# Performance work log

Hardware: AMD Instinct MI355X
Metric: run time of the kernel (lower is better)

## Reference

```python
import jax, jax.numpy as jnp
import numpy as np

N, T, D, H = 256, 512, 256, 256


def setup_inputs() -> dict:
    key = jax.random.key(0)
    ks = jax.random.split(key, 9)
    scale_x = float(np.sqrt(6.0 / (D + H)))  # xavier_uniform range approx
    scale_h = float(np.sqrt(6.0 / (H + H)))
    def wx(k):
        return jax.random.uniform(k, (D, H), jnp.float32, -scale_x, scale_x)
    def wh(k):
        return jax.random.uniform(k, (H, H), jnp.float32, -scale_h, scale_h)
    inp = {
        'x': jax.random.normal(ks[0], (N, T, D), jnp.float32),
        'w_ii': wx(ks[1]), 'w_hi': wh(ks[2]),
        'w_if': wx(ks[3]), 'w_hf': wh(ks[4]),
        'w_ig': wx(ks[5]), 'w_hg': wh(ks[6]),
        'w_io': wx(ks[7]), 'w_ho': wh(ks[8]),
        # init_hidden() zeros all 1-D params
        'b_ii': jnp.zeros((H,), jnp.float32), 'b_hi': jnp.zeros((H,), jnp.float32),
        'b_if': jnp.zeros((H,), jnp.float32), 'b_hf': jnp.zeros((H,), jnp.float32),
        'b_ig': jnp.zeros((H,), jnp.float32), 'b_hg': jnp.zeros((H,), jnp.float32),
        'b_io': jnp.zeros((H,), jnp.float32), 'b_ho': jnp.zeros((H,), jnp.float32),
    }
    return inp


def reference(x, w_ii, w_hi, w_if, w_hf, w_ig, w_hg, w_io, w_ho,
              b_ii, b_hi, b_if, b_hf, b_ig, b_hg, b_io, b_ho):
    # Fuse the 4 input projections and 4 hidden projections into 2 GEMMs
    # (mathematically identical to the 8 separate matmuls).
    Wx = jnp.concatenate([w_ii, w_if, w_ig, w_io], axis=1)  # (D, 4H)
    Wh = jnp.concatenate([w_hi, w_hf, w_hg, w_ho], axis=1)  # (H, 4H)
    b = jnp.concatenate([b_ii + b_hi, b_if + b_hf, b_ig + b_hg, b_io + b_ho])  # (4H,)
    n, t, _ = x.shape
    h = x.shape[2]  # noqa (not used)
    # Precompute input projections for all timesteps: (T, N, 4H)
    xW = jnp.einsum('ntd,dg->tng', x, Wx)
    h0 = jnp.zeros((n, w_hi.shape[0]), x.dtype)
    c0 = jnp.zeros_like(h0)

    def step(carry, xw_t):
        h_t, c_t = carry
        gates = xw_t + h_t @ Wh + b  # (N, 4H)
        i_t, f_t, g_t, o_t = jnp.split(gates, 4, axis=1)
        i_t = jax.nn.sigmoid(i_t)
        f_t = jax.nn.sigmoid(f_t)
        g_t = jnp.tanh(g_t)
        o_t = jax.nn.sigmoid(o_t)
        c_t = f_t * c_t + i_t * g_t
        h_t = o_t * jnp.tanh(c_t)
        return (h_t, c_t), None

    (h_T, c_T), _ = jax.lax.scan(step, (h0, c0), xW)
    return (h_T, c_T)
```

## Files before the change

kernel.cpp:

```cpp
#include <hip/hip_runtime.h>
#include <cstdint>

typedef float  f32x4  __attribute__((ext_vector_type(4)));
typedef __bf16 bf16x8 __attribute__((ext_vector_type(8)));
typedef int    i32x4  __attribute__((ext_vector_type(4)));
typedef unsigned short u16;
typedef u16 u16x4 __attribute__((ext_vector_type(4)));

#define TT 512

__device__ __forceinline__ u16 f2bf(float f) {
  unsigned u = __builtin_bit_cast(unsigned, f);
  unsigned r = u + 0x7fffu + ((u >> 16) & 1u);
  return (u16)(r >> 16);
}
__device__ __forceinline__ float bflo(unsigned d) { return __builtin_bit_cast(float, d << 16); }
__device__ __forceinline__ float bfhi(unsigned d) { return __builtin_bit_cast(float, d & 0xffff0000u); }
__device__ __forceinline__ float rcpf(float x) { return __builtin_amdgcn_rcpf(x); }
__device__ __forceinline__ float fsig(float x) { return rcpf(1.f + __expf(-x)); }
__device__ __forceinline__ float ftanh(float x) { return 1.f - 2.f * rcpf(1.f + __expf(2.f * x)); }
__device__ __forceinline__ void gload_lds16(const u16* g, u16* l) {
  __builtin_amdgcn_global_load_lds((const __attribute__((address_space(1))) void*)(g),
                                   (__attribute__((address_space(3))) void*)(l), 16, 0, 0);
}

__global__ __launch_bounds__(256) void prep_w(
    const float* __restrict__ wii, const float* __restrict__ whi,
    const float* __restrict__ wif, const float* __restrict__ whf,
    const float* __restrict__ wig, const float* __restrict__ whg,
    const float* __restrict__ wio, const float* __restrict__ who,
    const float* __restrict__ bii, const float* __restrict__ bhi,
    const float* __restrict__ bif, const float* __restrict__ bhf,
    const float* __restrict__ big_, const float* __restrict__ bhg,
    const float* __restrict__ bio, const float* __restrict__ bho,
    u16* __restrict__ Wxb, signed char* __restrict__ Whq,
    float* __restrict__ wscale, float* __restrict__ bsum) {
  __shared__ float red[256];
  int b = blockIdx.x;
  int tid = threadIdx.x;
  if (b < 1024) {
    const float* wx[4] = {wii, wif, wig, wio};
    int G = b >> 8, h = b & 255;
    Wxb[b * 256 + tid] = f2bf(wx[G][tid * 256 + h]);
  } else if (b < 2048) {
    const float* wh[4] = {whi, whf, whg, who};
    int cidx = b - 1024;
    int G = cidx >> 8, h = cidx & 255;
    float w = wh[G][tid * 256 + h];
    red[tid] = fabsf(w);
    __syncthreads();
    for (int s = 128; s > 0; s >>= 1) {
      if (tid < s) red[tid] = fmaxf(red[tid], red[tid + s]);
      __syncthreads();
    }
    float mx = red[0];
    float scale = (mx > 0.f) ? mx * (1.f / 127.f) : 1.f;
    float qf = rintf(w / scale);
    qf = fminf(127.f, fmaxf(-127.f, qf));
    Whq[cidx * 256 + tid] = (signed char)(int)qf;
    if (tid == 0) wscale[cidx] = scale * (1.f / 127.f);
  } else {
    const float* bx[4] = {bii, bif, big_, bio};
    const float* bh[4] = {bhi, bhf, bhg, bho};
    for (int G = 0; G < 4; ++G) bsum[G * 256 + tid] = bx[G][tid] + bh[G][tid];
  }
}

__global__ __launch_bounds__(256, 2) void gemm_xw(const float* __restrict__ X, const u16* __restrict__ Bt,
                                                  const float* __restrict__ bias, u16* __restrict__ xWp) {
  __shared__ u16 As[128 * 256];
  __shared__ u16 Bs[2][128 * 32];
  int bm = blockIdx.x;
  int tid = threadIdx.x;
  int l = tid & 63, w = tid >> 6;
  int wm = w >> 1, wn = w & 1;
  int c = l & 15, q = l >> 4;

  {
    int trow = tid >> 2, ch = tid & 3;
    gload_lds16(Bt + (size_t)trow * 256 + ch * 8, &Bs[0][0] + tid * 8);
    gload_lds16(Bt + (size_t)(trow + 64) * 256 + ch * 8, &Bs[0][0] + 2048 + tid * 8);
  }
  {
#pragma unroll 4
    for (int j = 0; j < 32; ++j) {
      int row_l = j * 4 + (tid >> 6);
      int d = (tid & 63) * 4;
      int r = bm * 128 + row_l;
      int t = r >> 8, n = r & 255;
      const float4 v = *(const float4*)(X + ((size_t)n * 512 + t) * 256 + d);
      u16x4 p;
      p[0] = f2bf(v.x); p[1] = f2bf(v.y); p[2] = f2bf(v.z); p[3] = f2bf(v.w);
      int ba = (row_l * 512 + d * 2) ^ ((row_l & 7) << 4);
      *(u16x4*)((char*)As + ba) = p;
    }
  }
  __syncthreads();

  f32x4 acc[4][4];
#pragma unroll
  for (int i = 0; i < 4; ++i)
#pragma unroll
    for (int j = 0; j < 4; ++j) acc[i][j] = (f32x4){0.f, 0.f, 0.f, 0.f};

  int sw = (c & 7) << 4;
  int rowbase[4];
#pragma unroll
  for (int mt = 0; mt < 4; ++mt)
    rowbase[mt] = (wm * 64 + mt * 16 + c) * 512;

  for (int bn = 0; bn < 8; ++bn) {
#pragma unroll
    for (int ko = 0; ko < 8; ++ko) {
      int sn = bn * 8 + ko + 1;
      if (sn < 64) {
        int bnn = sn >> 3, kon = sn & 7;
        const u16* Bb = Bt + (size_t)(bnn * 128) * 256 + kon * 32;
        u16* dst = &Bs[(ko + 1) & 1][0];
        int trow = tid >> 2, ch = tid & 3;
        gload_lds16(Bb + (size_t)trow * 256 + ch * 8, dst + tid * 8);
        gload_lds16(Bb + (size_t)(trow + 64) * 256 + ch * 8, dst + 2048 + tid * 8);
      }
      bf16x8 af[4], bfr[4];
      const u16* bp = &Bs[ko & 1][0];
      int koff = (ko * 64 + q * 16) ^ sw;
#pragma unroll
      for (int mt = 0; mt < 4; ++mt)
        af[mt] = *(const bf16x8*)((const char*)As + rowbase[mt] + koff);
#pragma unroll
      for (int nt = 0; nt < 4; ++nt)
        bfr[nt] = *(const bf16x8*)(bp + (wn * 64 + nt * 16 + c) * 32 + q * 8);
#pragma unroll
      for (int mt = 0; mt < 4; ++mt)
#pragma unroll
        for (int nt = 0; nt < 4; ++nt)
          acc[mt][nt] = __builtin_amdgcn_mfma_f32_16x16x32_bf16(af[mt], bfr[nt], acc[mt][nt], 0, 0, 0);
      __syncthreads();
    }
#pragma unroll
    for (int mt = 0; mt < 4; ++mt) {
      int tm = bm * 8 + wm * 4 + mt;
#pragma unroll
      for (int nt = 0; nt < 4; ++nt) {
        int tn = bn * 8 + wn * 4 + nt;
        float bv = bias[tn * 16 + c];
        u16x4 pk;
#pragma unroll
        for (int r = 0; r < 4; ++r) pk[r] = f2bf(acc[mt][nt][r] + bv);
        *reinterpret_cast<u16x4*>(xWp + ((size_t)(tm * 64 + tn) * 256 + l * 4)) = pk;
        acc[mt][nt] = (f32x4){0.f, 0.f, 0.f, 0.f};
      }
    }
  }
}

__global__ __launch_bounds__(512, 2) void lstm_rec(const signed char* __restrict__ Whq,
                                                   const float* __restrict__ wscale,
                                                   const u16* __restrict__ xWp,
                                                   float* __restrict__ out) {
  __shared__ __align__(16) signed char hb[2][576];
  int p = blockIdx.x;
  int xcd = p & 7, q8 = (p >> 3) & 7, tsel = p >> 6;
  int G = xcd * 2 + tsel;
  int tid = threadIdx.x;
  int wid = tid >> 6, l = tid & 63;
  int c = l & 15, q = (l >> 4) & 3;
  int tt = q >> 1, rsel = q & 1;

  for (int i = tid; i < 288; i += 512) ((int*)hb)[i] = 0;

  i32x4 bw[4][2][4];
#pragma unroll
  for (int g = 0; g < 4; ++g)
#pragma unroll
    for (int ttl = 0; ttl < 2; ++ttl) {
      int col = g * 256 + wid * 32 + ttl * 16 + c;
#pragma unroll
      for (int ks = 0; ks < 4; ++ks)
        bw[g][ttl][ks] = *reinterpret_cast<const i32x4*>(Whq + (size_t)col * 256 + ks * 64 + q * 16);
    }
  float sc8[4];
#pragma unroll
  for (int g = 0; g < 4; ++g) sc8[g] = wscale[g * 256 + wid * 32 + tt * 16 + c];

  const char* xbase = (const char*)xWp + (size_t)G * 32768;
  int xoff[4];
#pragma unroll
  for (int g = 0; g < 4; ++g) {
    int tn = g * 16 + wid * 2 + tt;
    xoff[g] = tn * 512 + (((q8 >> 1) * 16 + c) * 8) + (q8 & 1) * 4;
  }
  unsigned xw0[4], xw1[4];
#pragma unroll
  for (int g = 0; g < 4; ++g) xw0[g] = *(const unsigned*)(xbase + xoff[g]);
  xbase += 524288;

  i32x4 zacc = (i32x4){0, 0, 0, 0};
  float cs = 0.f, hh = 0.f;
  __syncthreads();

#define STEP(CUR, XW_CUR, XW_NXT)                                               \
  {                                                                             \
    _Pragma("unroll")                                                           \
    for (int g = 0; g < 4; ++g) XW_NXT[g] = *(const unsigned*)(xbase + xoff[g]);\
    const signed char* hr = hb[CUR ^ 1];                                        \
    i32x4 acc[4][2];                                                            \
    {                                                                           \
      i32x4 a0 = *(const i32x4*)(hr + (c & 1) * 288 + q * 16);                  \
      _Pragma("unroll")                                                         \
      for (int g = 0; g < 4; ++g) {                                             \
        __asm__("v_mfma_i32_16x16x64_i8 %0, %1, %2, %3"                         \
                : "=&v"(acc[g][0]) : "v"(a0), "a"(bw[g][0][0]), "v"(zacc));     \
        __asm__("v_mfma_i32_16x16x64_i8 %0, %1, %2, %3"                         \
                : "=&v"(acc[g][1]) : "v"(a0), "a"(bw[g][1][0]), "v"(zacc));     \
      }                                                                         \
    }                                                                           \
    _Pragma("unroll")                                                           \
    for (int ks = 1; ks < 4; ++ks) {                                            \
      i32x4 a = *(const i32x4*)(hr + (c & 1) * 288 + ks * 64 + q * 16);         \
      _Pragma("unroll")                                                         \
      for (int g = 0; g < 4; ++g) {                                             \
        __asm__("v_mfma_i32_16x16x64_i8 %0, %1, %2, %0"                         \
                : "+v"(acc[g][0]) : "v"(a), "a"(bw[g][0][ks]));                 \
        __asm__("v_mfma_i32_16x16x64_i8 %0, %1, %2, %0"                         \
                : "+v"(acc[g][1]) : "v"(a), "a"(bw[g][1][ks]));                 \
      }                                                                         \
    }                                                                           \
    __asm__ volatile("s_nop 7\n\ts_nop 7\n\ts_nop 7");   \
    float a4[4];                                                                \
    _Pragma("unroll")                                                           \
    for (int g = 0; g < 4; ++g) {                                               \
      int e = tt ? (rsel ? acc[g][1][1] : acc[g][1][0])                         \
                 : (rsel ? acc[g][0][1] : acc[g][0][0]);                        \
      unsigned d = XW_CUR[g];                                                   \
      float xv = rsel ? bfhi(d) : bflo(d);                                      \
      a4[g] = (float)e * sc8[g] + xv;                                           \
    }                                                                           \
    float gi = fsig(a4[0]);                                                     \
    float gf = fsig(a4[1]);                                                     \
    float gg = ftanh(a4[2]);                                                    \
    float go = fsig(a4[3]);                                                     \
    cs = gf * cs + gi * gg;                                                     \
    hh = go * ftanh(cs);                                                        \
    int hq = (int)rintf(hh * 127.f);                                            \
    hb[CUR][rsel * 288 + wid * 32 + tt * 16 + c] = (signed char)hq;             \
    xbase += 524288;                                                            \
    __builtin_amdgcn_s_waitcnt(0xC07F);   \
    __builtin_amdgcn_s_barrier();                                               \
  }

  for (int t = 0; t < TT; t += 2) {
    STEP(0, xw0, xw1)
    STEP(1, xw1, xw0)
  }
#undef STEP

  {
    int n = G * 16 + q8 * 2 + rsel;
    int hu = wid * 32 + tt * 16 + c;
    out[(size_t)n * 256 + hu] = hh;
    out[65536 + (size_t)n * 256 + hu] = cs;
  }
}

extern "C" void kernel_launch(void* const* d_in, const int* in_sizes, int n_in,
                              void* d_out, int out_size, void* d_ws, size_t ws_size,
                              hipStream_t stream) {
  const float* x   = (const float*)d_in[0];
  const float* wii = (const float*)d_in[1];
  const float* whi = (const float*)d_in[2];
  const float* wif = (const float*)d_in[3];
  const float* whf = (const float*)d_in[4];
  const float* wig = (const float*)d_in[5];
  const float* whg = (const float*)d_in[6];
  const float* wio = (const float*)d_in[7];
  const float* who = (const float*)d_in[8];
  const float* bii = (const float*)d_in[9];
  const float* bhi = (const float*)d_in[10];
  const float* bif = (const float*)d_in[11];
  const float* bhf = (const float*)d_in[12];
  const float* big_ = (const float*)d_in[13];
  const float* bhg = (const float*)d_in[14];
  const float* bio = (const float*)d_in[15];
  const float* bho = (const float*)d_in[16];

  char* ws = (char*)d_ws;
  u16*   Wxb    = (u16*)(ws + 67108864);
  signed char* Whq = (signed char*)(ws + 67633152);
  float* wscale = (float*)(ws + 67895296);
  float* bsum   = (float*)(ws + 67899392);
  u16*   xWp    = (u16*)(ws + 67903488);
  float* out = (float*)d_out;

  prep_w<<<2049, 256, 0, stream>>>(wii, whi, wif, whf, wig, whg, wio, who,
                                   bii, bhi, bif, bhf, big_, bhg, bio, bho,
                                   Wxb, Whq, wscale, bsum);
  gemm_xw<<<1024, 256, 0, stream>>>(x, Wxb, bsum, xWp);
  lstm_rec<<<128, 512, 0, stream>>>(Whq, wscale, xWp, out);
}
```

Baseline: 692.0 us.

## Fuse input GEMM and recurrence into one kernel with per-chunk progress flags

Merges the input-projection GEMM and the LSTM recurrence into a single launch. 128 blocks run the recurrence and 128 blocks compute xW in chunks of 64 timesteps, publishing completion through atomic counters. Recurrence blocks spin-wait on each chunk's counter before consuming it, so the GEMM overlaps with the serial recurrence instead of running before it. This relies on all 256 blocks being co-resident, adds spin-wait and barrier overhead, and gives the recurrence blocks the GEMM's large LDS footprint.

```diff
diff --git a/kernel.cpp b/kernel.cpp
--- a/kernel.cpp
+++ b/kernel.cpp
@@ -66,103 +66,103 @@
   }
 }
 
-__global__ __launch_bounds__(256, 2) void gemm_xw(const float* __restrict__ X, const u16* __restrict__ Bt,
-                                                  const float* __restrict__ bias, u16* __restrict__ xWp) {
+__global__ __launch_bounds__(512, 2) void lstm_fused(
+    const float* __restrict__ X, const u16* __restrict__ Bt,
+    const float* __restrict__ bias, const signed char* __restrict__ Whq,
+    const float* __restrict__ wscale, u16* __restrict__ xWp,
+    int* __restrict__ rprog, float* __restrict__ out) {
   __shared__ u16 As[128 * 256];
   __shared__ u16 Bs[2][128 * 32];
-  int bm = blockIdx.x;
-  int tid = threadIdx.x;
-  int l = tid & 63, w = tid >> 6;
-  int wm = w >> 1, wn = w & 1;
-  int c = l & 15, q = l >> 4;
-
-  {
-    int trow = tid >> 2, ch = tid & 3;
-    gload_lds16(Bt + (size_t)trow * 256 + ch * 8, &Bs[0][0] + tid * 8);
-    gload_lds16(Bt + (size_t)(trow + 64) * 256 + ch * 8, &Bs[0][0] + 2048 + tid * 8);
-  }
-  {
-#pragma unroll 4
-    for (int j = 0; j < 32; ++j) {
-      int row_l = j * 4 + (tid >> 6);
-      int d = (tid & 63) * 4;
-      int r = bm * 128 + row_l;
-      int t = r >> 8, n = r & 255;
-      const float4 v = *(const float4*)(X + ((size_t)n * 512 + t) * 256 + d);
-      u16x4 p;
-      p[0] = f2bf(v.x); p[1] = f2bf(v.y); p[2] = f2bf(v.z); p[3] = f2bf(v.w);
-      int ba = (row_l * 512 + d * 2) ^ ((row_l & 7) << 4);
-      *(u16x4*)((char*)As + ba) = p;
-    }
-  }
-  __syncthreads();
-
-  f32x4 acc[4][4];
-#pragma unroll
-  for (int i = 0; i < 4; ++i)
-#pragma unroll
-    for (int j = 0; j < 4; ++j) acc[i][j] = (f32x4){0.f, 0.f, 0.f, 0.f};
-
-  int sw = (c & 7) << 4;
-  int rowbase[4];
-#pragma unroll
-  for (int mt = 0; mt < 4; ++mt)
-    rowbase[mt] = (wm * 64 + mt * 16 + c) * 512;
-
-  for (int bn = 0; bn < 8; ++bn) {
-#pragma unroll
-    for (int ko = 0; ko < 8; ++ko) {
-      int sn = bn * 8 + ko + 1;
-      if (sn < 64) {
-        int bnn = sn >> 3, kon = sn & 7;
-        const u16* Bb = Bt + (size_t)(bnn * 128) * 256 + kon * 32;
-        u16* dst = &Bs[(ko + 1) & 1][0];
-        int trow = tid >> 2, ch = tid & 3;
-        gload_lds16(Bb + (size_t)trow * 256 + ch * 8, dst + tid * 8);
-        gload_lds16(Bb + (size_t)(trow + 64) * 256 + ch * 8, dst + 2048 + tid * 8);
-      }
-      bf16x8 af[4], bfr[4];
-      const u16* bp = &Bs[ko & 1][0];
-      int koff = (ko * 64 + q * 16) ^ sw;
-#pragma unroll
-      for (int mt = 0; mt < 4; ++mt)
-        af[mt] = *(const bf16x8*)((const char*)As + rowbase[mt] + koff);
-#pragma unroll
-      for (int nt = 0; nt < 4; ++nt)
-        bfr[nt] = *(const bf16x8*)(bp + (wn * 64 + nt * 16 + c) * 32 + q * 8);
-#pragma unroll
-      for (int mt = 0; mt < 4; ++mt)
-#pragma unroll
-        for (int nt = 0; nt < 4; ++nt)
-          acc[mt][nt] = __builtin_amdgcn_mfma_f32_16x16x32_bf16(af[mt], bfr[nt], acc[mt][nt], 0, 0, 0);
-      __syncthreads();
-    }
-#pragma unroll
-    for (int mt = 0; mt < 4; ++mt) {
-      int tm = bm * 8 + wm * 4 + mt;
-#pragma unroll
-      for (int nt = 0; nt < 4; ++nt) {
-        int tn = bn * 8 + wn * 4 + nt;
-        float bv = bias[tn * 16 + c];
-        u16x4 pk;
-#pragma unroll
-        for (int r = 0; r < 4; ++r) pk[r] = f2bf(acc[mt][nt][r] + bv);
-        *reinterpret_cast<u16x4*>(xWp + ((size_t)(tm * 64 + tn) * 256 + l * 4)) = pk;
-        acc[mt][nt] = (f32x4){0.f, 0.f, 0.f, 0.f};
-      }
-    }
-  }
-}
-
-__global__ __launch_bounds__(512, 2) void lstm_rec(const signed char* __restrict__ Whq,
-                                                   const float* __restrict__ wscale,
-                                                   const u16* __restrict__ xWp,
-                                                   float* __restrict__ out) {
   __shared__ __align__(16) signed char hb[2][576];
   int p = blockIdx.x;
+  int tid = threadIdx.x;
+
+  if (p >= 128) {
+    int k = p - 128;
+    int l = tid & 63, w8 = tid >> 6;
+    int wm = w8 >> 2, wn = w8 & 3;
+    int c = l & 15, q = l >> 4;
+    int sw = (c & 7) << 4;
+    int rowbase[4];
+#pragma unroll
+    for (int mt = 0; mt < 4; ++mt) rowbase[mt] = (wm * 64 + mt * 16 + c) * 512;
+
+    for (int j = 0; j < 8; ++j) {
+      int bm = j * 128 + k;
+      {
+        int trow = tid >> 2, ch = tid & 3;
+        gload_lds16(Bt + (size_t)trow * 256 + ch * 8, &Bs[0][0] + tid * 8);
+      }
+#pragma unroll 4
+      for (int jj = 0; jj < 16; ++jj) {
+        int row_l = jj * 8 + w8;
+        int d = l * 4;
+        int r = bm * 128 + row_l;
+        int t = r >> 8, n = r & 255;
+        const float4 v = *(const float4*)(X + ((size_t)n * 512 + t) * 256 + d);
+        u16x4 pk;
+        pk[0] = f2bf(v.x); pk[1] = f2bf(v.y); pk[2] = f2bf(v.z); pk[3] = f2bf(v.w);
+        int ba = (row_l * 512 + l * 8) ^ ((row_l & 7) << 4);
+        *(u16x4*)((char*)As + ba) = pk;
+      }
+      __syncthreads();
+
+      f32x4 acc[4][2];
+#pragma unroll
+      for (int i = 0; i < 4; ++i)
+#pragma unroll
+        for (int jn = 0; jn < 2; ++jn) acc[i][jn] = (f32x4){0.f, 0.f, 0.f, 0.f};
+
+      for (int bn = 0; bn < 8; ++bn) {
+#pragma unroll
+        for (int ko = 0; ko < 8; ++ko) {
+          int sn = bn * 8 + ko + 1;
+          if (sn < 64) {
+            int bnn = sn >> 3, kon = sn & 7;
+            const u16* Bb = Bt + (size_t)(bnn * 128) * 256 + kon * 32;
+            int trow = tid >> 2, ch = tid & 3;
+            gload_lds16(Bb + (size_t)trow * 256 + ch * 8, &Bs[(ko + 1) & 1][0] + tid * 8);
+          }
+          bf16x8 af[4], bfr[2];
+          const u16* bp = &Bs[ko & 1][0];
+          int koff = (ko * 64 + q * 16) ^ sw;
+#pragma unroll
+          for (int mt = 0; mt < 4; ++mt)
+            af[mt] = *(const bf16x8*)((const char*)As + rowbase[mt] + koff);
+#pragma unroll
+          for (int nt = 0; nt < 2; ++nt)
+            bfr[nt] = *(const bf16x8*)(bp + (wn * 32 + nt * 16 + c) * 32 + q * 8);
+#pragma unroll
+          for (int mt = 0; mt < 4; ++mt)
+#pragma unroll
+            for (int nt = 0; nt < 2; ++nt)
+              acc[mt][nt] = __builtin_amdgcn_mfma_f32_16x16x32_bf16(af[mt], bfr[nt], acc[mt][nt], 0, 0, 0);
+          __syncthreads();
+        }
+#pragma unroll
+        for (int mt = 0; mt < 4; ++mt) {
+          int tm = bm * 8 + wm * 4 + mt;
+#pragma unroll
+          for (int nt = 0; nt < 2; ++nt) {
+            int tn = bn * 8 + wn * 2 + nt;
+            float bv = bias[tn * 16 + c];
+            u16x4 pk;
+#pragma unroll
+            for (int r = 0; r < 4; ++r) pk[r] = f2bf(acc[mt][nt][r] + bv);
+            *reinterpret_cast<u16x4*>(xWp + ((size_t)(tm * 64 + tn) * 256 + l * 4)) = pk;
+            acc[mt][nt] = (f32x4){0.f, 0.f, 0.f, 0.f};
+          }
+        }
+      }
+      __syncthreads();
+      if (tid == 0)
+        __hip_atomic_fetch_add(&rprog[j], 1, __ATOMIC_RELEASE, __HIP_MEMORY_SCOPE_AGENT);
+    }
+    return;
+  }
+
   int xcd = p & 7, q8 = (p >> 3) & 7, tsel = p >> 6;
   int G = xcd * 2 + tsel;
-  int tid = threadIdx.x;
   int wid = tid >> 6, l = tid & 63;
   int c = l & 15, q = (l >> 4) & 3;
   int tt = q >> 1, rsel = q & 1;
@@ -190,6 +190,14 @@
     int tn = g * 16 + wid * 2 + tt;
     xoff[g] = tn * 512 + (((q8 >> 1) * 16 + c) * 8) + (q8 & 1) * 4;
   }
+
+  if (tid == 0) {
+    while (__hip_atomic_load(&rprog[0], __ATOMIC_RELAXED, __HIP_MEMORY_SCOPE_AGENT) < 128)
+      __builtin_amdgcn_s_sleep(8);
+    (void)__hip_atomic_load(&rprog[0], __ATOMIC_ACQUIRE, __HIP_MEMORY_SCOPE_AGENT);
+  }
+  __syncthreads();
+
   unsigned xw0[4], xw1[4];
 #pragma unroll
   for (int g = 0; g < 4; ++g) xw0[g] = *(const unsigned*)(xbase + xoff[g]);
@@ -251,6 +259,15 @@
 
   for (int t = 0; t < TT; t += 2) {
     STEP(0, xw0, xw1)
+    if (((t + 2) & 63) == 0 && (t + 2) < TT) {
+      int j = (t + 2) >> 6;
+      if (tid == 0) {
+        while (__hip_atomic_load(&rprog[j], __ATOMIC_RELAXED, __HIP_MEMORY_SCOPE_AGENT) < 128)
+          __builtin_amdgcn_s_sleep(8);
+        (void)__hip_atomic_load(&rprog[j], __ATOMIC_ACQUIRE, __HIP_MEMORY_SCOPE_AGENT);
+      }
+      __syncthreads();
+    }
     STEP(1, xw1, xw0)
   }
 #undef STEP
@@ -285,6 +302,7 @@
   const float* bho = (const float*)d_in[16];
 
   char* ws = (char*)d_ws;
+  int*   rprog  = (int*)(ws);
   u16*   Wxb    = (u16*)(ws + 67108864);
   signed char* Whq = (signed char*)(ws + 67633152);
   float* wscale = (float*)(ws + 67895296);
@@ -292,9 +310,9 @@
   u16*   xWp    = (u16*)(ws + 67903488);
   float* out = (float*)d_out;
 
+  hipMemsetAsync(rprog, 0, 64, stream);
   prep_w<<<2049, 256, 0, stream>>>(wii, whi, wif, whf, wig, whg, wio, who,
                                    bii, bhi, bif, bhf, big_, bhg, bio, bho,
                                    Wxb, Whq, wscale, bsum);
-  gemm_xw<<<1024, 256, 0, stream>>>(x, Wxb, bsum, xWp);
-  lstm_rec<<<128, 512, 0, stream>>>(Whq, wscale, xWp, out);
-}
+  lstm_fused<<<256, 512, 0, stream>>>(x, Wxb, bsum, Whq, wscale, xWp, rprog, out);
+}
```

Result: faster. 637.7 us (-7.9%).
